# Kernel tuning notes

Measured on AMD Instinct MI355X. Metric: run time of the kernel, lower is better.

The kernel has to match this reference:

```python
import jax, jax.numpy as jnp
import numpy as np
import math

N_EMBED = 512
ENC_HEADS = 8
DEC_HEADS = 16          # 2 * config.n_head
HEAD_DIM = N_EMBED // DEC_HEADS  # 32
N_LAYER = 2
N_MELS = 80
N_AUDIO_CTX = 750
N_TEXT_CTX = 448
VOCAB = 51865
OPT_VOCAB = (VOCAB + 63) // 64 * 64  # 51904
PAD_ID = 0
B = 4
L = 448


def rms(x, eps=1e-6):
    return x * jax.lax.rsqrt(jnp.mean(x * x, axis=-1, keepdims=True) + eps)


def _rotary_tables(T, hd, base=10000.0):
    inv = 1.0 / (base ** (np.arange(0, hd, 2, dtype=np.float64) / hd))
    f = np.arange(T, dtype=np.float64)[:, None] * inv[None, :]
    cos = np.cos(f)[None, :, None, :].astype(np.float32)  # (1,T,1,hd/2)
    sin = np.sin(f)[None, :, None, :].astype(np.float32)
    return jnp.asarray(cos), jnp.asarray(sin)

ROPE_COS, ROPE_SIN = _rotary_tables(10 * N_TEXT_CTX, HEAD_DIM)


def apply_rope(x, cos, sin):
    # x: (b, L, h, hd); cos/sin: (1, L, 1, hd/2)
    d = x.shape[-1] // 2
    x1, x2 = x[..., :d], x[..., d:]
    return jnp.concatenate([x1 * cos + x2 * sin, -x1 * sin + x2 * cos], axis=-1)


def sinusoids(length, channels, max_timescale=10000.0):
    inc = math.log(max_timescale) / (channels // 2 - 1)
    invt = np.exp(-inc * np.arange(channels // 2))
    st = np.arange(length)[:, None] * invt[None, :]
    return jnp.asarray(np.concatenate([np.sin(st), np.cos(st)], axis=1), jnp.float32)

ENC_POS = sinusoids(N_AUDIO_CTX, N_EMBED)


def linear(x, w, b=None):
    y = jnp.einsum('...i,oi->...o', x, w)
    return y + b if b is not None else y


def heads(x, h):
    b, l, _ = x.shape
    return x.reshape(b, l, h, -1).transpose(0, 2, 1, 3)  # (b,h,l,hd)


def conv1d(x, w, b, stride):
    y = jax.lax.conv_general_dilated(x, w, (stride,), [(1, 1)],
                                     dimension_numbers=('NCH', 'OIH', 'NCH'))
    return y + b[None, :, None]


def attn(q, k, v, mask, decorrelate):
    # q,k,v: (b,h,l,hd)
    scale = 1.0 / math.sqrt(q.shape[-1])
    s = jnp.einsum('bhqd,bhkd->bhqk', q, k) * scale
    if mask is not None:
        s = s + mask
    a = jax.nn.softmax(s, axis=-1)
    o = jnp.einsum('bhqk,bhkd->bhqd', a, v)
    if decorrelate:
        # subtract projection of output onto L2-normalized v (self_attn branch)
        vn = v / jnp.maximum(jnp.linalg.norm(v, axis=-1, keepdims=True), 1e-9)
        o = o - jnp.sum(o * vn, axis=-1, keepdims=True) * vn
    b, h, l, d = o.shape
    return o.transpose(0, 2, 1, 3).reshape(b, l, h * d)


def _forward(input_ids, mels, conv1_w, conv1_b, conv2_w, conv2_b,
             enc_qw, enc_qb, enc_kw, enc_kb, enc_vw, enc_vb, enc_ow, enc_ob,
             enc_fcw, enc_fcb, enc_pjw, enc_pjb,
             sqw, sqb, skw, skb, svw, svb, sow, sob,
             cqw, cqb, ckw, ckb, cvw, cvb, cow, cob,
             fcw, fcb, pjw, pjb, embed_w, pos_embed):
    b, Lq = input_ids.shape
    # ---------- audio encoder (Whisper-style convs + custom attn blocks) ----------
    x = jax.nn.gelu(conv1d(mels, conv1_w, conv1_b, 1), approximate=False)
    x = jax.nn.gelu(conv1d(x, conv2_w, conv2_b, 2), approximate=False)
    x = x.transpose(0, 2, 1) + ENC_POS[None]  # (B, n_audio_ctx, n_embed)
    for i in range(N_LAYER):
        h = rms(x)
        q = rms(heads(linear(h, enc_qw[i], enc_qb[i]), ENC_HEADS))
        k = rms(heads(linear(h, enc_kw[i], enc_kb[i]), ENC_HEADS))
        v = heads(linear(h, enc_vw[i], enc_vb[i]), ENC_HEADS)
        x = x + linear(attn(q, k, v, None, True), enc_ow[i], enc_ob[i])
        x = x + linear(jax.nn.gelu(linear(rms(x), enc_fcw[i], enc_fcb[i]), approximate=False),
                       enc_pjw[i], enc_pjb[i])
    aud = rms(x)
    # cross-attn kv projection of audio (no rope)
    aud_k = rms(heads(linear(aud, ckw, ckb), DEC_HEADS))
    aud_v = heads(linear(aud, cvw, cvb), DEC_HEADS)

    # ---------- decoder ----------
    cos, sin = ROPE_COS[:, :Lq], ROPE_SIN[:, :Lq]
    q0 = jnp.broadcast_to(pos_embed[:, :Lq], (b, Lq, N_EMBED))
    ctx = embed_w[input_ids] * math.sqrt(N_EMBED)
    ctx = jnp.concatenate([ctx[:, :1], ctx[:, 1:] + pos_embed[:, :Lq - 1]], axis=1)
    ctx = rms(ctx)

    # self-attn projections: rope then qk-norm; k uses shifted cos/sin
    qh = linear(rms(q0), sqw, sqb).reshape(b, Lq, DEC_HEADS, HEAD_DIM)
    qh = rms(apply_rope(qh, cos, sin).transpose(0, 2, 1, 3))
    k_cos = jnp.concatenate([cos[:, :1], cos[:, :-1]], axis=1)
    k_sin = jnp.concatenate([sin[:, :1], sin[:, :-1]], axis=1)
    kh = linear(ctx, skw, skb).reshape(b, Lq, DEC_HEADS, HEAD_DIM)
    kh = rms(apply_rope(kh, k_cos, k_sin).transpose(0, 2, 1, 3))
    vh = heads(linear(ctx, svw, svb), DEC_HEADS)

    causal = jnp.triu(jnp.full((Lq, Lq), -jnp.inf, jnp.float32), 1)
    kpm = jnp.where(input_ids == PAD_ID, -jnp.inf, 0.0).astype(jnp.float32)
    mask = causal[None, None] + kpm[:, None, None, :]  # (b,1,Lq,Lq)

    res = q0 + linear(attn(qh, kh, vh, mask, True), sow, sob)

    # cross attention (rope on q only, no v-decorrelation)
    q2 = linear(rms(res), cqw, cqb).reshape(b, Lq, DEC_HEADS, HEAD_DIM)
    q2 = rms(apply_rope(q2, cos, sin).transpose(0, 2, 1, 3))
    res = res + linear(attn(q2, aud_k, aud_v, None, False), cow, cob)
    res = res + linear(jax.nn.gelu(linear(rms(res), fcw, fcb), approximate=False), pjw, pjb)

    logits = linear(rms(res), embed_w)  # tied lm head, no bias
    return logits.astype(jnp.float32)


def setup_inputs():
    key = jax.random.key(0)
    ks = iter(jax.random.split(key, 64))
    def w(shape, std=0.02):
        return jax.random.normal(next(ks), shape, jnp.float32) * std
    d = {}
    d['mels'] = jax.random.normal(next(ks), (B, N_MELS, 2 * N_AUDIO_CTX), jnp.float32)
    d['input_ids'] = jax.random.randint(next(ks), (B, L), 1, VOCAB)
    d['conv1_w'] = w((N_EMBED, N_MELS, 3)); d['conv1_b'] = jnp.zeros((N_EMBED,), jnp.float32)
    d['conv2_w'] = w((N_EMBED, N_EMBED, 3)); d['conv2_b'] = jnp.zeros((N_EMBED,), jnp.float32)
    for nm in ['enc_qw', 'enc_kw', 'enc_vw', 'enc_ow']:
        d[nm] = w((N_LAYER, N_EMBED, N_EMBED)); d[nm[:-1] + 'b'] = jnp.zeros((N_LAYER, N_EMBED), jnp.float32)
    d['enc_fcw'] = w((N_LAYER, 4 * N_EMBED, N_EMBED)); d['enc_fcb'] = jnp.zeros((N_LAYER, 4 * N_EMBED), jnp.float32)
    d['enc_pjw'] = w((N_LAYER, N_EMBED, 4 * N_EMBED)); d['enc_pjb'] = jnp.zeros((N_LAYER, N_EMBED), jnp.float32)
    for nm in ['sqw', 'skw', 'svw', 'sow', 'cqw', 'ckw', 'cvw', 'cow']:
        d[nm] = w((N_EMBED, N_EMBED)); d[nm[:-1] + 'b'] = jnp.zeros((N_EMBED,), jnp.float32)
    d['fcw'] = w((4 * N_EMBED, N_EMBED)); d['fcb'] = jnp.zeros((4 * N_EMBED,), jnp.float32)
    d['pjw'] = w((N_EMBED, 4 * N_EMBED)); d['pjb'] = jnp.zeros((N_EMBED,), jnp.float32)
    d['embed_w'] = w((OPT_VOCAB, N_EMBED))
    d['pos_embed'] = jax.random.normal(next(ks), (1, N_TEXT_CTX, N_EMBED), jnp.float32)
    return d


def reference(mels, input_ids, conv1_w, conv1_b, conv2_w, conv2_b,
              enc_qw, enc_qb, enc_kw, enc_kb, enc_vw, enc_vb, enc_ow, enc_ob,
              enc_fcw, enc_fcb, enc_pjw, enc_pjb,
              sqw, sqb, skw, skb, svw, svb, sow, sob,
              cqw, cqb, ckw, ckb, cvw, cvb, cow, cob,
              fcw, fcb, pjw, pjb, embed_w, pos_embed):
    return _forward(input_ids, mels, conv1_w, conv1_b, conv2_w, conv2_b,
                    enc_qw, enc_qb, enc_kw, enc_kb, enc_vw, enc_vb, enc_ow, enc_ob,
                    enc_fcw, enc_fcb, enc_pjw, enc_pjb,
                    sqw, sqb, skw, skb, svw, svb, sow, sob,
                    cqw, cqb, ckw, ckb, cvw, cvb, cow, cob,
                    fcw, fcb, pjw, pjb, embed_w, pos_embed)
```

## Files before the change

### kernel.cpp

```cpp
#include <hip/hip_runtime.h>
#include <math.h>

#define CDIV(a,b) (((a)+(b)-1)/(b))

static constexpr int NE  = 512;
static constexpr int EH  = 8;
static constexpr int EHD = 64;
static constexpr int DHN = 16;
static constexpr int HDD = 32;
static constexpr int NM  = 80;
static constexpr int TMl = 1500;
static constexpr int TP  = 1502;
static constexpr int TA  = 750;
static constexpr int LQ  = 448;
static constexpr int NB  = 4;
static constexpr int OV  = 51904;

typedef __attribute__((ext_vector_type(8))) short bf16x8;
typedef __attribute__((ext_vector_type(8))) unsigned short us8;
typedef __attribute__((ext_vector_type(4))) float f32x4;


__global__ void k_transpose_mels(const float* __restrict__ mels, float* __restrict__ melsT) {
    long idx = (long)blockIdx.x * blockDim.x + threadIdx.x;
    long total = (long)NB * TP * NM;
    if (idx >= total) return;
    int ci = (int)(idx % NM);
    int t  = (int)((idx / NM) % TP);
    int b  = (int)(idx / ((long)NM * TP));
    float v = 0.f;
    if (t >= 1 && t <= TMl) v = mels[((long)b * NM + ci) * TMl + (t - 1)];
    melsT[idx] = v;
}

__global__ void k_zero_x1t_pads(float* __restrict__ x1t) {
    int idx = blockIdx.x * blockDim.x + threadIdx.x;
    if (idx >= NB * 2 * NE) return;
    int c = idx % NE;
    int r = (idx / NE) % 2;
    int b = idx / (NE * 2);
    int t = r ? (TP - 1) : 0;
    x1t[((long)b * TP + t) * NE + c] = 0.f;
}

__global__ void k_repack_w(const float* __restrict__ w, float* __restrict__ wr, int O, int I) {
    long idx = (long)blockIdx.x * blockDim.x + threadIdx.x;
    long total = (long)O * I * 3;
    if (idx >= total) return;
    int k = (int)(idx % 3);
    int i = (int)((idx / 3) % I);
    int o = (int)(idx / ((long)3 * I));
    wr[(long)o * (3 * I) + k * I + i] = w[idx];
}

__global__ void k_add_encpos(float* __restrict__ x) {
    long idx = (long)blockIdx.x * blockDim.x + threadIdx.x;
    long total = (long)NB * TA * NE;
    if (idx >= total) return;
    int c = (int)(idx % NE);
    int t = (int)((idx / NE) % TA);
    double inc = log(10000.0) / 255.0;
    int j = c & 255;
    double st = (double)t * exp(-inc * (double)j);
    float p = (c < 256) ? (float)sin(st) : (float)cos(st);
    x[idx] += p;
}

__global__ void k_embed(const int* __restrict__ ids, const float* __restrict__ ew,
                        const float* __restrict__ pos, float* __restrict__ ctx) {
    long idx = (long)blockIdx.x * blockDim.x + threadIdx.x;
    long total = (long)NB * LQ * NE;
    if (idx >= total) return;
    int c = (int)(idx % NE);
    int t = (int)((idx / NE) % LQ);
    int b = (int)(idx / ((long)NE * LQ));
    int id = ids[b * LQ + t];
    float v = ew[(long)id * NE + c] * 22.62741699796952f;
    if (t >= 1) v += pos[(long)(t - 1) * NE + c];
    ctx[idx] = v;
}

__global__ void k_bcast_pos(const float* __restrict__ pos, float* __restrict__ dst, int Bn) {
    long idx = (long)blockIdx.x * blockDim.x + threadIdx.x;
    long total = (long)Bn * LQ * NE;
    if (idx >= total) return;
    int c = (int)(idx % NE);
    int t = (int)((idx / NE) % LQ);
    dst[idx] = pos[(long)t * NE + c];
}

__global__ void k_ropetab(float* __restrict__ ctab, float* __restrict__ stab) {
    int idx = blockIdx.x * blockDim.x + threadIdx.x;
    if (idx >= LQ * 16) return;
    int m = idx % 16;
    int t = idx / 16;
    double inv = pow(10000.0, -(double)(2 * m) / 32.0);
    double f = (double)t * inv;
    ctab[idx] = (float)cos(f);
    stab[idx] = (float)sin(f);
}

__global__ void k_rope(float* __restrict__ x, int Bn, int shiftK, int RS,
                       const float* __restrict__ ctab, const float* __restrict__ stab) {
    long idx = (long)blockIdx.x * blockDim.x + threadIdx.x;
    long total = (long)Bn * LQ * DHN * 16;
    if (idx >= total) return;
    int m = (int)(idx % 16);
    int h = (int)((idx / 16) % DHN);
    int t = (int)((idx / (16 * DHN)) % LQ);
    int b = (int)(idx / ((long)16 * DHN * LQ));
    int tt = shiftK ? (t > 0 ? t - 1 : 0) : t;
    float c = ctab[tt * 16 + m];
    float s = stab[tt * 16 + m];
    long base = ((long)b * LQ + t) * RS + h * HDD;
    float x1 = x[base + m];
    float x2 = x[base + 16 + m];
    x[base + m]      = x1 * c + x2 * s;
    x[base + 16 + m] = -x1 * s + x2 * c;
}


__global__ void k_rms512(const float* __restrict__ src, float* __restrict__ dst, int rows) {
    int wave = blockIdx.x * (blockDim.x >> 6) + (threadIdx.x >> 6);
    int lane = threadIdx.x & 63;
    if (wave >= rows) return;
    const float* s = src + (long)wave * NE;
    float4 a = *(const float4*)(s + lane * 4);
    float4 b = *(const float4*)(s + 256 + lane * 4);
    float ss = a.x*a.x + a.y*a.y + a.z*a.z + a.w*a.w
             + b.x*b.x + b.y*b.y + b.z*b.z + b.w*b.w;
    for (int m = 32; m >= 1; m >>= 1) ss += __shfl_xor(ss, m, 64);
    float sc = rsqrtf(ss / 512.f + 1e-6f);
    float* d = dst + (long)wave * NE;
    a.x *= sc; a.y *= sc; a.z *= sc; a.w *= sc;
    b.x *= sc; b.y *= sc; b.z *= sc; b.w *= sc;
    *(float4*)(d + lane * 4) = a;
    *(float4*)(d + 256 + lane * 4) = b;
}

template<int D>
__global__ void k_rms_heads(float* __restrict__ x, long nchunks, int CU, int RS) {
    const int RPW = 64 / D;
    long wave = (long)blockIdx.x * (blockDim.x >> 6) + (threadIdx.x >> 6);
    int lane = threadIdx.x & 63;
    long rr = wave * RPW + lane / D;
    if (rr >= nchunks) return;
    int col = lane % D;
    long idx = (rr / CU) * (long)RS + (rr % CU) * D + col;
    float v = x[idx];
    float ss = v * v;
    for (int m = D / 2; m >= 1; m >>= 1) ss += __shfl_xor(ss, m, 64);
    x[idx] = v * rsqrtf(ss / (float)D + 1e-6f);
}

template<int D>
__global__ void k_decorrelate(float* __restrict__ o, const float* __restrict__ v,
                              long nchunks, int CU, int vRS, int vOff) {
    const int RPW = 64 / D;
    long wave = (long)blockIdx.x * (blockDim.x >> 6) + (threadIdx.x >> 6);
    int lane = threadIdx.x & 63;
    long rr = wave * RPW + lane / D;
    if (rr >= nchunks) return;
    int col = lane % D;
    long oidx = rr * D + col;
    long vidx = (rr / CU) * (long)vRS + vOff + (rr % CU) * D + col;
    float ov = o[oidx];
    float vv = v[vidx];
    float dov = ov * vv;
    float dvv = vv * vv;
    for (int m = D / 2; m >= 1; m >>= 1) {
        dov += __shfl_xor(dov, m, 64);
        dvv += __shfl_xor(dvv, m, 64);
    }
    float nv = sqrtf(dvv);
    float c = fmaxf(nv, 1e-9f);
    o[oidx] = ov - (dov / (c * c)) * vv;
}

__global__ void k_softmax(float* __restrict__ s, int H, int Lq, int Lk,
                          int causal, const int* __restrict__ ids, long nrows) {
    long row = (long)blockIdx.x * (blockDim.x >> 6) + (threadIdx.x >> 6);
    if (row >= nrows) return;
    int lane = threadIdx.x & 63;
    int qt = (int)(row % Lq);
    long z = row / Lq;
    int b = (int)(z / H);
    float* p = s + row * (long)Lk;
    int cnt = (Lk + 63) >> 6;
    float vals[12];
    float mx = -INFINITY;
    for (int i = 0; i < cnt; i++) {
        int k = lane + (i << 6);
        float v = -INFINITY;
        if (k < Lk) {
            v = p[k];
            if (causal && k > qt) v = -INFINITY;
            if (ids && ids[(long)b * Lk + k] == 0) v = -INFINITY;
        }
        vals[i] = v;
        mx = fmaxf(mx, v);
    }
    for (int m = 32; m >= 1; m >>= 1) mx = fmaxf(mx, __shfl_xor(mx, m, 64));
    float sum = 0.f;
    for (int i = 0; i < cnt; i++) {
        float e = expf(vals[i] - mx);
        vals[i] = e;
        sum += e;
    }
    for (int m = 32; m >= 1; m >>= 1) sum += __shfl_xor(sum, m, 64);
    float inv = 1.f / sum;
    for (int i = 0; i < cnt; i++) {
        int k = lane + (i << 6);
        if (k < Lk) p[k] = vals[i] * inv;
    }
}


template<bool TRANSB>
__global__ __launch_bounds__(256) void k_gemm(
    const float* __restrict__ A, const float* __restrict__ Bm,
    const float* __restrict__ bias, float* __restrict__ C,
    int M, int N, int K, int lda, int ldb, int ldc,
    long sAb, long sAh, long sBb, long sBh, long sCb, long sCh, int H,
    float alpha, float beta, int act)
{
    __shared__ __align__(16) float As[16][68];
    __shared__ __align__(16) float Bs[16][68];
    int z = blockIdx.z;
    int bb = z / H, hh = z % H;
// ... 79 lines not shown
                                             sAb, sAh, sBb, sBh, sCb, sCh, H, alpha, beta, act);
}


__global__ __launch_bounds__(256, 4) void k_gemm_mf(
    const float* __restrict__ A, const float* __restrict__ B,
    const float* __restrict__ bias, float* __restrict__ C,
    int M, int N, int K, int lda, int ldb, int ldc,
    long sAb, long sAh, long sBb, long sBh, long sCb, long sCh, int H,
    int gx, int gy, float alpha, float beta, int act)
{
    __shared__ __align__(16) unsigned short lds[16384];
    int nwg = gridDim.x;
    int flat = blockIdx.x;
    int q8 = nwg >> 3, r8 = nwg & 7;
    int xcd = flat & 7, idx = flat >> 3;
    int wg = (xcd < r8 ? xcd * (q8 + 1) : r8 * (q8 + 1) + (xcd - r8) * q8) + idx;
    int my = wg % gy;
    int t2 = wg / gy;
    int nx = t2 % gx;
    int z  = t2 / gx;
    int bb = z / H, hh = z % H;
    A += (long)bb * sAb + (long)hh * sAh;
    B += (long)bb * sBb + (long)hh * sBh;
    C += (long)bb * sCb + (long)hh * sCh;
    int m0 = my * 128, n0 = nx * 128;
    const int tid = threadIdx.x;
    const int wid = tid >> 6, lane = tid & 63;
    const int wm = wid >> 1, wn = wid & 1;
    const int lr = lane & 15, lk = lane >> 4;
    const int rA = tid >> 2, g = tid & 3;

    f32x4 acc[4][4] = {};

    for (int k0 = 0; k0 < K; k0 += 32) {
        __syncthreads();
        int kk = k0 + g * 8;
        bool kv = kk < K;
        #pragma unroll
        for (int half = 0; half < 2; ++half) {
            int r = rA + half * 64;
            int off = r * 32 + (g ^ ((r >> 1) & 3)) * 8;
            {
                float4 f0 = {0,0,0,0}, f1 = {0,0,0,0};
                if (kv && m0 + r < M) {
                    const float* p = A + (long)(m0 + r) * lda + kk;
                    f0 = *(const float4*)p;
                    f1 = *(const float4*)(p + 4);
                }
                float ff[8] = {f0.x,f0.y,f0.z,f0.w,f1.x,f1.y,f1.z,f1.w};
                us8 h, l;
                #pragma unroll
                for (int j = 0; j < 8; ++j) {
                    unsigned bu = __float_as_uint(ff[j]);
                    unsigned hb = bu & 0xffff0000u;
                    h[j] = (unsigned short)(hb >> 16);
                    l[j] = (unsigned short)(__float_as_uint(ff[j] - __uint_as_float(hb)) >> 16);
                }
                *(us8*)(lds + off) = h;
                *(us8*)(lds + 4096 + off) = l;
            }
            {
                float4 f0 = {0,0,0,0}, f1 = {0,0,0,0};
                if (kv && n0 + r < N) {
                    const float* p = B + (long)(n0 + r) * ldb + kk;
                    f0 = *(const float4*)p;
                    f1 = *(const float4*)(p + 4);
                }
                float ff[8] = {f0.x,f0.y,f0.z,f0.w,f1.x,f1.y,f1.z,f1.w};
                us8 h, l;
                #pragma unroll
                for (int j = 0; j < 8; ++j) {
                    unsigned bu = __float_as_uint(ff[j]);
                    unsigned hb = bu & 0xffff0000u;
                    h[j] = (unsigned short)(hb >> 16);
                    l[j] = (unsigned short)(__float_as_uint(ff[j] - __uint_as_float(hb)) >> 16);
                }
                *(us8*)(lds + 8192 + off) = h;
                *(us8*)(lds + 12288 + off) = l;
            }
        }
        __syncthreads();
        bf16x8 ah[4], al[4];
        #pragma unroll
        for (int i = 0; i < 4; ++i) {
            int ra = wm * 64 + i * 16 + lr;
            int ao = ra * 32 + (lk ^ ((ra >> 1) & 3)) * 8;
            ah[i] = *(const bf16x8*)(lds + ao);
            al[i] = *(const bf16x8*)(lds + 4096 + ao);
        }
        #pragma unroll
        for (int j = 0; j < 4; ++j) {
            int rb = wn * 64 + j * 16 + lr;
            int bo = rb * 32 + (lk ^ ((rb >> 1) & 3)) * 8;
            bf16x8 bh = *(const bf16x8*)(lds + 8192 + bo);
            bf16x8 bl = *(const bf16x8*)(lds + 12288 + bo);
            #pragma unroll
            for (int i = 0; i < 4; ++i) {
                acc[i][j] = __builtin_amdgcn_mfma_f32_16x16x32_bf16(ah[i], bh, acc[i][j], 0, 0, 0);
                acc[i][j] = __builtin_amdgcn_mfma_f32_16x16x32_bf16(ah[i], bl, acc[i][j], 0, 0, 0);
                acc[i][j] = __builtin_amdgcn_mfma_f32_16x16x32_bf16(al[i], bh, acc[i][j], 0, 0, 0);
            }
        }
    }
    #pragma unroll
    for (int i = 0; i < 4; ++i) {
        int rowb = m0 + wm * 64 + i * 16 + lk * 4;
        #pragma unroll
        for (int j = 0; j < 4; ++j) {
            int col = n0 + wn * 64 + j * 16 + lr;
            if (col >= N) continue;
            float bi = bias ? bias[col] : 0.f;
            #pragma unroll
            for (int qi = 0; qi < 4; ++qi) {
                int row = rowb + qi;
                if (row >= M) continue;
                float v = alpha * acc[i][j][qi] + bi;
                long off = (long)row * ldc + col;
                if (beta != 0.f) v += beta * C[off];
                if (act) v = 0.5f * v * (1.f + erff(v * 0.70710678118654752f));
                C[off] = v;
            }
        }
    }
}

static inline void gemm_mf(hipStream_t st, const float* A, const float* B, const float* bias,
                           float* C, int M, int N, int K, int lda, int ldb, int ldc,
                           long sAb, long sAh, long sBb, long sBh, long sCb, long sCh,
                           int Z, int H, float alpha, float beta, int act)
{
    int gx = CDIV(N, 128), gy = CDIV(M, 128);
    dim3 g((unsigned)(gx * gy * Z));
    k_gemm_mf<<<g, 256, 0, st>>>(A, B, bias, C, M, N, K, lda, ldb, ldc,
                                 sAb, sAh, sBb, sBh, sCb, sCh, H, gx, gy, alpha, beta, act);
}


extern "C" void kernel_launch(void* const* d_in, const int* in_sizes, int n_in,
                              void* d_out, int out_size, void* d_ws, size_t ws_size,
                              hipStream_t stream)
{
    const float* mels = (const float*)d_in[0];
    const int*   ids  = (const int*)  d_in[1];
    const float* c1w  = (const float*)d_in[2];
    const float* c1b  = (const float*)d_in[3];
    const float* c2w  = (const float*)d_in[4];
    const float* c2b  = (const float*)d_in[5];
    const float* eqw  = (const float*)d_in[6];
    const float* eqb  = (const float*)d_in[7];
    const float* ekw  = (const float*)d_in[8];
    const float* ekb  = (const float*)d_in[9];
    const float* evw  = (const float*)d_in[10];
    const float* evb  = (const float*)d_in[11];
    const float* eow  = (const float*)d_in[12];
    const float* eob  = (const float*)d_in[13];
    const float* efcw = (const float*)d_in[14];
    const float* efcb = (const float*)d_in[15];
    const float* epjw = (const float*)d_in[16];
    const float* epjb = (const float*)d_in[17];
    const float* sqw  = (const float*)d_in[18];
    const float* sqb  = (const float*)d_in[19];
    const float* skw  = (const float*)d_in[20];
    const float* skb  = (const float*)d_in[21];
    const float* svw  = (const float*)d_in[22];
    const float* svb  = (const float*)d_in[23];
    const float* soww = (const float*)d_in[24];
    const float* sob  = (const float*)d_in[25];
    const float* cqw  = (const float*)d_in[26];
    const float* cqb  = (const float*)d_in[27];
    const float* ckw  = (const float*)d_in[28];
    const float* ckb  = (const float*)d_in[29];
    const float* cvw  = (const float*)d_in[30];
    const float* cvb  = (const float*)d_in[31];
    const float* coww = (const float*)d_in[32];
    const float* cob  = (const float*)d_in[33];
    const float* fcw  = (const float*)d_in[34];
    const float* fcb  = (const float*)d_in[35];
    const float* pjw  = (const float*)d_in[36];
    const float* pjb  = (const float*)d_in[37];
    const float* embw = (const float*)d_in[38];
    const float* pose = (const float*)d_in[39];
    float* out = (float*)d_out;

    float* ws = (float*)d_ws;
    long off = 0;
    auto alloc = [&](long n) { float* p = ws + off; off += n; return p; };
    float* melsT = alloc((long)NB * TP * NM);
    float* x1t   = alloc((long)NB * TP * NE);
    float* w1r   = alloc(3L * NE * NM);
    float* w2r   = alloc(3L * NE * NE);
    float* xenc  = alloc((long)NB * TA * NE);
    float* hbuf  = alloc((long)NB * TA * NE);
    float* qbuf  = alloc((long)NB * TA * NE);
    float* kbuf  = alloc((long)NB * TA * NE);
    float* vbuf  = alloc((long)NB * TA * NE);
    float* obuf  = alloc((long)NB * TA * NE);
    float* fcbuf = alloc((long)NB * TA * 2048);
    float* sc    = alloc((long)NB * DHN * LQ * TA);
    float* audk  = alloc((long)NB * TA * NE);
    float* audv  = alloc((long)NB * TA * NE);
    float* ctx   = alloc((long)NB * LQ * NE);
    float* q0r   = alloc((long)LQ * NE);
    float* qh    = alloc((long)NB * LQ * NE);
    float* kh    = alloc((long)NB * LQ * NE);
    float* vh    = alloc((long)NB * LQ * NE);
    float* res   = alloc((long)NB * LQ * NE);
    float* t1    = alloc((long)NB * LQ * NE);
    float* odec  = alloc((long)NB * LQ * NE);
    float* ctab  = alloc((long)LQ * 16);
    float* stab  = alloc((long)LQ * 16);
    float* cbias = alloc(2048);
    (void)ws_size; (void)in_sizes; (void)n_in; (void)out_size;
    (void)qbuf; (void)kbuf; (void)vbuf; (void)audk; (void)audv; (void)kh; (void)vh;

    const int MA = NB * TA;
    const int MD = NB * LQ;
    const float dscale = 0.17677669529663687f;

    float* selfkv = fcbuf;
    float* audkv  = fcbuf + 3000000L;

    auto dcopy = [&](float* dst, const float* src, long n) {
        hipMemcpyAsync(dst, src, n * sizeof(float), hipMemcpyDeviceToDevice, stream);
    };

    k_transpose_mels<<<CDIV((long)NB * TP * NM, 256), 256, 0, stream>>>(mels, melsT);
    k_repack_w<<<CDIV(3L * NE * NM, 256), 256, 0, stream>>>(c1w, w1r, NE, NM);
    k_repack_w<<<CDIV(3L * NE * NE, 256), 256, 0, stream>>>(c2w, w2r, NE, NE);
    k_zero_x1t_pads<<<CDIV(NB * 2 * NE, 256), 256, 0, stream>>>(x1t);
    gemm_mf(stream, melsT, w1r, c1b, x1t + NE,
            TMl, NE, 3 * NM, NM, 3 * NM, NE,
            (long)TP * NM, 0, 0, 0, (long)TP * NE, 0, NB, 1, 1.f, 0.f, 1);
    gemm_mf(stream, x1t, w2r, c2b, xenc,
            TA, NE, 3 * NE, 2 * NE, 3 * NE, NE,
            (long)TP * NE, 0, 0, 0, (long)TA * NE, 0, NB, 1, 1.f, 0.f, 1);
    k_add_encpos<<<CDIV((long)NB * TA * NE, 256), 256, 0, stream>>>(xenc);

    for (int l = 0; l < 2; l++) {
        const float* qw = eqw + (long)l * NE * NE; const float* qb = eqb + l * NE;
        const float* kw = ekw + (long)l * NE * NE; const float* kb = ekb + l * NE;
        const float* vw = evw + (long)l * NE * NE; const float* vb = evb + l * NE;
        const float* ow = eow + (long)l * NE * NE; const float* ob = eob + l * NE;
        const float* fw = efcw + (long)l * 2048 * NE; const float* fb = efcb + l * 2048;
        const float* pw = epjw + (long)l * NE * 2048; const float* pb = epjb + l * NE;

        dcopy(w2r,                   qw, (long)NE * NE);
        dcopy(w2r + (long)NE * NE,   kw, (long)NE * NE);
        dcopy(w2r + 2L * NE * NE,    vw, (long)NE * NE);
        dcopy(cbias,        qb, NE);
        dcopy(cbias + NE,   kb, NE);
        dcopy(cbias + 2*NE, vb, NE);

        k_rms512<<<CDIV(MA, 4), 256, 0, stream>>>(xenc, hbuf, MA);
        gemm_mf(stream, hbuf, w2r, cbias, fcbuf, MA, 3 * NE, NE, NE, NE, 3 * NE,
                0,0,0,0,0,0, 1,1, 1.f, 0.f, 0);
        k_rms_heads<64><<<CDIV((long)MA * 16, 4), 256, 0, stream>>>(fcbuf, (long)MA * 16, 16, 3 * NE);
        gemm_mf(stream, fcbuf, fcbuf + NE, nullptr, sc, TA, TA, EHD, 3 * NE, 3 * NE, TA,
                (long)TA * 3 * NE, EHD, (long)TA * 3 * NE, EHD, (long)EH * TA * TA, (long)TA * TA,
                NB * EH, EH, 0.125f, 0.f, 0);
        k_softmax<<<CDIV((long)NB * EH * TA, 4), 256, 0, stream>>>(sc, EH, TA, TA, 0, nullptr, (long)NB * EH * TA);
        gemm(stream, false, sc, fcbuf + 2 * NE, nullptr, obuf, TA, EHD, TA, TA, 3 * NE, NE,
             (long)EH * TA * TA, (long)TA * TA, (long)TA * 3 * NE, EHD, (long)TA * NE, EHD,
             NB * EH, EH, 1.f, 0.f, 0);
        k_decorrelate<64><<<CDIV((long)MA * EH, 4), 256, 0, stream>>>(obuf, fcbuf + 2 * NE, (long)MA * EH, EH, 3 * NE, 0);
        gemm_mf(stream, obuf, ow, ob, xenc, MA, NE, NE, NE, NE, NE, 0,0,0,0,0,0, 1,1, 1.f, 1.f, 0);

        k_rms512<<<CDIV(MA, 4), 256, 0, stream>>>(xenc, hbuf, MA);
        gemm_mf(stream, hbuf, fw, fb, fcbuf, MA, 2048, NE, NE, NE, 2048, 0,0,0,0,0,0, 1,1, 1.f, 0.f, 1);
        gemm_mf(stream, fcbuf, pw, pb, xenc, MA, NE, 2048, 2048, 2048, NE, 0,0,0,0,0,0, 1,1, 1.f, 1.f, 0);
    }

    dcopy(w2r,                 ckw, (long)NE * NE);
    dcopy(w2r + (long)NE * NE, cvw, (long)NE * NE);
    dcopy(cbias,      ckb, NE);
    dcopy(cbias + NE, cvb, NE);
    k_rms512<<<CDIV(MA, 4), 256, 0, stream>>>(xenc, hbuf, MA);
    gemm_mf(stream, hbuf, w2r, cbias, audkv, MA, 2 * NE, NE, NE, NE, 2 * NE,
            0,0,0,0,0,0, 1,1, 1.f, 0.f, 0);
    k_rms_heads<32><<<CDIV((long)MA * DHN, 8), 256, 0, stream>>>(audkv, (long)MA * DHN, DHN, 2 * NE);

    k_embed<<<CDIV((long)NB * LQ * NE, 256), 256, 0, stream>>>(ids, embw, pose, ctx);
    k_rms512<<<CDIV(MD, 4), 256, 0, stream>>>(ctx, ctx, MD);
    k_ropetab<<<CDIV(LQ * 16, 256), 256, 0, stream>>>(ctab, stab);

    k_bcast_pos<<<CDIV((long)LQ * NE, 256), 256, 0, stream>>>(pose, q0r, 1);
    k_rms512<<<CDIV(LQ, 4), 256, 0, stream>>>(q0r, q0r, LQ);
    gemm_mf(stream, q0r, sqw, sqb, qh, LQ, NE, NE, NE, NE, NE, 0,0,0,0,0,0, 1,1, 1.f, 0.f, 0);
    k_rope<<<CDIV((long)LQ * DHN * 16, 256), 256, 0, stream>>>(qh, 1, 0, NE, ctab, stab);
    k_rms_heads<32><<<CDIV((long)LQ * DHN, 8), 256, 0, stream>>>(qh, (long)LQ * DHN, DHN, NE);

    dcopy(w2r,                 skw, (long)NE * NE);
    dcopy(w2r + (long)NE * NE, svw, (long)NE * NE);
    dcopy(cbias,      skb, NE);
    dcopy(cbias + NE, svb, NE);
    gemm_mf(stream, ctx, w2r, cbias, selfkv, MD, 2 * NE, NE, NE, NE, 2 * NE,
            0,0,0,0,0,0, 1,1, 1.f, 0.f, 0);
    k_rope<<<CDIV((long)NB * LQ * DHN * 16, 256), 256, 0, stream>>>(selfkv, NB, 1, 2 * NE, ctab, stab);
    k_rms_heads<32><<<CDIV((long)MD * DHN, 8), 256, 0, stream>>>(selfkv, (long)MD * DHN, DHN, 2 * NE);

    gemm_mf(stream, qh, selfkv, nullptr, sc, LQ, LQ, HDD, NE, 2 * NE, LQ,
            0, HDD, (long)LQ * 2 * NE, HDD, (long)DHN * LQ * LQ, (long)LQ * LQ,
            NB * DHN, DHN, dscale, 0.f, 0);
    k_softmax<<<CDIV((long)NB * DHN * LQ, 4), 256, 0, stream>>>(sc, DHN, LQ, LQ, 1, ids, (long)NB * DHN * LQ);
    gemm(stream, false, sc, selfkv + NE, nullptr, odec, LQ, HDD, LQ, LQ, 2 * NE, NE,
         (long)DHN * LQ * LQ, (long)LQ * LQ, (long)LQ * 2 * NE, HDD, (long)LQ * NE, HDD,
         NB * DHN, DHN, 1.f, 0.f, 0);
    k_decorrelate<32><<<CDIV((long)MD * DHN, 8), 256, 0, stream>>>(odec, selfkv + NE, (long)MD * DHN, DHN, 2 * NE, 0);
    k_bcast_pos<<<CDIV((long)NB * LQ * NE, 256), 256, 0, stream>>>(pose, res, NB);
    gemm_mf(stream, odec, soww, sob, res, MD, NE, NE, NE, NE, NE, 0,0,0,0,0,0, 1,1, 1.f, 1.f, 0);

    k_rms512<<<CDIV(MD, 4), 256, 0, stream>>>(res, t1, MD);
    gemm_mf(stream, t1, cqw, cqb, qh, MD, NE, NE, NE, NE, NE, 0,0,0,0,0,0, 1,1, 1.f, 0.f, 0);
    k_rope<<<CDIV((long)NB * LQ * DHN * 16, 256), 256, 0, stream>>>(qh, NB, 0, NE, ctab, stab);
    k_rms_heads<32><<<CDIV((long)MD * DHN, 8), 256, 0, stream>>>(qh, (long)MD * DHN, DHN, NE);
    gemm_mf(stream, qh, audkv, nullptr, sc, LQ, TA, HDD, NE, 2 * NE, TA,
            (long)LQ * NE, HDD, (long)TA * 2 * NE, HDD, (long)DHN * LQ * TA, (long)LQ * TA,
            NB * DHN, DHN, dscale, 0.f, 0);
    k_softmax<<<CDIV((long)NB * DHN * LQ, 4), 256, 0, stream>>>(sc, DHN, LQ, TA, 0, nullptr, (long)NB * DHN * LQ);
    gemm(stream, false, sc, audkv + NE, nullptr, odec, LQ, HDD, TA, TA, 2 * NE, NE,
         (long)DHN * LQ * TA, (long)LQ * TA, (long)TA * 2 * NE, HDD, (long)LQ * NE, HDD,
         NB * DHN, DHN, 1.f, 0.f, 0);
    gemm_mf(stream, odec, coww, cob, res, MD, NE, NE, NE, NE, NE, 0,0,0,0,0,0, 1,1, 1.f, 1.f, 0);

    k_rms512<<<CDIV(MD, 4), 256, 0, stream>>>(res, t1, MD);
    gemm_mf(stream, t1, fcw, fcb, fcbuf, MD, 2048, NE, NE, NE, 2048, 0,0,0,0,0,0, 1,1, 1.f, 0.f, 1);
    gemm_mf(stream, fcbuf, pjw, pjb, res, MD, NE, 2048, 2048, 2048, NE, 0,0,0,0,0,0, 1,1, 1.f, 1.f, 0);

    k_rms512<<<CDIV(MD, 4), 256, 0, stream>>>(res, t1, MD);
    gemm_mf(stream, t1, embw, nullptr, out, MD, OV, NE, NE, NE, OV,
            0,0,0,0,0,0, 1,1, 1.f, 0.f, 0);
}
```

Baseline: 3.214 ms.

## Pre-split operands into bf16 hi/lo buffers and add a split-input GEMM

```diff
diff --git a/kernel.cpp b/kernel.cpp
--- a/kernel.cpp
+++ b/kernel.cpp
@@ -20,8 +20,17 @@
 typedef __attribute__((ext_vector_type(8))) unsigned short us8;
 typedef __attribute__((ext_vector_type(4))) float f32x4;
 
-
-__global__ void k_transpose_mels(const float* __restrict__ mels, float* __restrict__ melsT) {
+__device__ __forceinline__ void split1(float f, unsigned short& h, unsigned short& l) {
+    unsigned bu = __float_as_uint(f);
+    unsigned hb = bu & 0xffff0000u;
+    h = (unsigned short)(hb >> 16);
+    l = (unsigned short)(__float_as_uint(f - __uint_as_float(hb)) >> 16);
+}
+
+
+__global__ void k_transpose_mels_s(const float* __restrict__ mels,
+                                   unsigned short* __restrict__ hi,
+                                   unsigned short* __restrict__ lo) {
     long idx = (long)blockIdx.x * blockDim.x + threadIdx.x;
     long total = (long)NB * TP * NM;
     if (idx >= total) return;
@@ -30,27 +39,33 @@
     int b  = (int)(idx / ((long)NM * TP));
     float v = 0.f;
     if (t >= 1 && t <= TMl) v = mels[((long)b * NM + ci) * TMl + (t - 1)];
-    melsT[idx] = v;
-}
-
-__global__ void k_zero_x1t_pads(float* __restrict__ x1t) {
+    unsigned short h, l; split1(v, h, l);
+    hi[idx] = h; lo[idx] = l;
+}
+
+__global__ void k_zero_x1t_pads_s(unsigned short* __restrict__ hi, unsigned short* __restrict__ lo) {
     int idx = blockIdx.x * blockDim.x + threadIdx.x;
     if (idx >= NB * 2 * NE) return;
     int c = idx % NE;
     int r = (idx / NE) % 2;
     int b = idx / (NE * 2);
     int t = r ? (TP - 1) : 0;
-    x1t[((long)b * TP + t) * NE + c] = 0.f;
-}
-
-__global__ void k_repack_w(const float* __restrict__ w, float* __restrict__ wr, int O, int I) {
+    long o = ((long)b * TP + t) * NE + c;
+    hi[o] = 0; lo[o] = 0;
+}
+
+__global__ void k_repack_w_s(const float* __restrict__ w,
+                             unsigned short* __restrict__ hi, unsigned short* __restrict__ lo,
+                             int O, int I) {
     long idx = (long)blockIdx.x * blockDim.x + threadIdx.x;
     long total = (long)O * I * 3;
     if (idx >= total) return;
     int k = (int)(idx % 3);
     int i = (int)((idx / 3) % I);
     int o = (int)(idx / ((long)3 * I));
-    wr[(long)o * (3 * I) + k * I + i] = w[idx];
+    unsigned short h, l; split1(w[idx], h, l);
+    long d = (long)o * (3 * I) + k * I + i;
+    hi[d] = h; lo[d] = l;
 }
 
 __global__ void k_add_encpos(float* __restrict__ x) {
@@ -120,7 +135,9 @@
 }
 
 
-__global__ void k_rms512(const float* __restrict__ src, float* __restrict__ dst, int rows) {
+__global__ void k_rms512s(const float* __restrict__ src,
+                          unsigned short* __restrict__ hi, unsigned short* __restrict__ lo,
+                          int rows) {
     int wave = blockIdx.x * (blockDim.x >> 6) + (threadIdx.x >> 6);
     int lane = threadIdx.x & 63;
     if (wave >= rows) return;
@@ -131,11 +148,18 @@
              + b.x*b.x + b.y*b.y + b.z*b.z + b.w*b.w;
     for (int m = 32; m >= 1; m >>= 1) ss += __shfl_xor(ss, m, 64);
     float sc = rsqrtf(ss / 512.f + 1e-6f);
-    float* d = dst + (long)wave * NE;
-    a.x *= sc; a.y *= sc; a.z *= sc; a.w *= sc;
-    b.x *= sc; b.y *= sc; b.z *= sc; b.w *= sc;
-    *(float4*)(d + lane * 4) = a;
-    *(float4*)(d + 256 + lane * 4) = b;
+    float fa[4] = {a.x*sc, a.y*sc, a.z*sc, a.w*sc};
+    float fb[4] = {b.x*sc, b.y*sc, b.z*sc, b.w*sc};
+    ushort4 ha, la, hb, lb;
+    split1(fa[0], ha.x, la.x); split1(fa[1], ha.y, la.y);
+    split1(fa[2], ha.z, la.z); split1(fa[3], ha.w, la.w);
+    split1(fb[0], hb.x, lb.x); split1(fb[1], hb.y, lb.y);
+    split1(fb[2], hb.z, lb.z); split1(fb[3], hb.w, lb.w);
+    long base = (long)wave * NE;
+    *(ushort4*)(hi + base + lane * 4) = ha;
+    *(ushort4*)(lo + base + lane * 4) = la;
+    *(ushort4*)(hi + base + 256 + lane * 4) = hb;
+    *(ushort4*)(lo + base + 256 + lane * 4) = lb;
 }
 
 template<int D>
@@ -154,8 +178,9 @@
 }
 
 template<int D>
-__global__ void k_decorrelate(float* __restrict__ o, const float* __restrict__ v,
-                              long nchunks, int CU, int vRS, int vOff) {
+__global__ void k_decorr_s(const float* __restrict__ o, const float* __restrict__ v,
+                           unsigned short* __restrict__ hi, unsigned short* __restrict__ lo,
+                           long nchunks, int CU, int vRS, int vOff) {
     const int RPW = 64 / D;
     long wave = (long)blockIdx.x * (blockDim.x >> 6) + (threadIdx.x >> 6);
     int lane = threadIdx.x & 63;
@@ -174,7 +199,22 @@
     }
     float nv = sqrtf(dvv);
     float c = fmaxf(nv, 1e-9f);
-    o[oidx] = ov - (dov / (c * c)) * vv;
+    float res = ov - (dov / (c * c)) * vv;
+    unsigned short h, l; split1(res, h, l);
+    hi[oidx] = h; lo[oidx] = l;
+}
+
+__global__ void k_split(const float* __restrict__ x, unsigned short* __restrict__ hi,
+                        unsigned short* __restrict__ lo, long n4)
+{
+    long i = (long)blockIdx.x * blockDim.x + threadIdx.x;
+    if (i >= n4) return;
+    float4 v = ((const float4*)x)[i];
+    ushort4 h, l;
+    split1(v.x, h.x, l.x); split1(v.y, h.y, l.y);
+    split1(v.z, h.z, l.z); split1(v.w, h.w, l.w);
+    ((ushort4*)hi)[i] = h;
+    ((ushort4*)lo)[i] = l;
 }
 
 __global__ void k_softmax(float* __restrict__ s, int H, int Lq, int Lk,
@@ -360,10 +400,8 @@
                 us8 h, l;
                 #pragma unroll
                 for (int j = 0; j < 8; ++j) {
-                    unsigned bu = __float_as_uint(ff[j]);
-                    unsigned hb = bu & 0xffff0000u;
-                    h[j] = (unsigned short)(hb >> 16);
-                    l[j] = (unsigned short)(__float_as_uint(ff[j] - __uint_as_float(hb)) >> 16);
+                    unsigned short hh2, ll2; split1(ff[j], hh2, ll2);
+                    h[j] = hh2; l[j] = ll2;
                 }
                 *(us8*)(lds + off) = h;
                 *(us8*)(lds + 4096 + off) = l;
@@ -379,10 +417,8 @@
                 us8 h, l;
                 #pragma unroll
                 for (int j = 0; j < 8; ++j) {
-                    unsigned bu = __float_as_uint(ff[j]);
-                    unsigned hb = bu & 0xffff0000u;
-                    h[j] = (unsigned short)(hb >> 16);
-                    l[j] = (unsigned short)(__float_as_uint(ff[j] - __uint_as_float(hb)) >> 16);
+                    unsigned short hh2, ll2; split1(ff[j], hh2, ll2);
+                    h[j] = hh2; l[j] = ll2;
                 }
                 *(us8*)(lds + 8192 + off) = h;
                 *(us8*)(lds + 12288 + off) = l;
@@ -442,6 +478,125 @@
     dim3 g((unsigned)(gx * gy * Z));
     k_gemm_mf<<<g, 256, 0, st>>>(A, B, bias, C, M, N, K, lda, ldb, ldc,
                                  sAb, sAh, sBb, sBh, sCb, sCh, H, gx, gy, alpha, beta, act);
+}
+
+
+__global__ __launch_bounds__(256, 4) void k_gemm_bs(
+    const unsigned short* __restrict__ Ah, const unsigned short* __restrict__ Al,
+    const unsigned short* __restrict__ Bh, const unsigned short* __restrict__ Bl,
+    const float* __restrict__ bias, float* __restrict__ C,
+    unsigned short* __restrict__ Chi, unsigned short* __restrict__ Clo,
+    int M, int N, int K, int lda, int ldb, int ldc,
+    long sAb, long sCb, int gx, int gy, float beta, int act, int osplit)
+{
+    __shared__ __align__(16) unsigned short lds[16384];
+    int nwg = gridDim.x;
+    int flat = blockIdx.x;
+    int q8 = nwg >> 3, r8 = nwg & 7;
+    int xcd = flat & 7, idx = flat >> 3;
+    int wg = (xcd < r8 ? xcd * (q8 + 1) : r8 * (q8 + 1) + (xcd - r8) * q8) + idx;
+    int my = wg % gy;
+    int t2 = wg / gy;
+    int nx = t2 % gx;
+    int bb = t2 / gx;
+    Ah += (long)bb * sAb; Al += (long)bb * sAb;
+    int m0 = my * 128, n0 = nx * 128;
+    const int tid = threadIdx.x;
+    const int wid = tid >> 6, lane = tid & 63;
+    const int wm = wid >> 1, wn = wid & 1;
+    const int lr = lane & 15, lk = lane >> 4;
+    const int rA = tid >> 2, g = tid & 3;
+
+    f32x4 acc[4][4] = {};
+
+    for (int k0 = 0; k0 < K; k0 += 32) {
+        __syncthreads();
+        int kk = k0 + g * 8;
+        bool kv = kk < K;
+        #pragma unroll
+        for (int half = 0; half < 2; ++half) {
+            int r = rA + half * 64;
+            int off = r * 32 + (g ^ ((r >> 1) & 3)) * 8;
+            us8 vh = {0,0,0,0,0,0,0,0}, vl = {0,0,0,0,0,0,0,0};
+            if (kv && m0 + r < M) {
+                long ao = (long)(m0 + r) * lda + kk;
+                vh = *(const us8*)(Ah + ao);
+                vl = *(const us8*)(Al + ao);
+            }
+            *(us8*)(lds + off) = vh;
+            *(us8*)(lds + 4096 + off) = vl;
+            us8 wh = {0,0,0,0,0,0,0,0}, wl = {0,0,0,0,0,0,0,0};
+            if (kv && n0 + r < N) {
+                long bo = (long)(n0 + r) * ldb + kk;
+                wh = *(const us8*)(Bh + bo);
+                wl = *(const us8*)(Bl + bo);
+            }
+            *(us8*)(lds + 8192 + off) = wh;
+            *(us8*)(lds + 12288 + off) = wl;
+        }
+        __syncthreads();
+        bf16x8 ah[4], al[4];
+        #pragma unroll
+        for (int i = 0; i < 4; ++i) {
+            int ra = wm * 64 + i * 16 + lr;
+            int ao = ra * 32 + (lk ^ ((ra >> 1) & 3)) * 8;
+            ah[i] = *(const bf16x8*)(lds + ao);
+            al[i] = *(const bf16x8*)(lds + 4096 + ao);
+        }
+        #pragma unroll
+        for (int j = 0; j < 4; ++j) {
+            int rb = wn * 64 + j * 16 + lr;
+            int bo = rb * 32 + (lk ^ ((rb >> 1) & 3)) * 8;
+            bf16x8 bh = *(const bf16x8*)(lds + 8192 + bo);
+            bf16x8 bl = *(const bf16x8*)(lds + 12288 + bo);
+            #pragma unroll
+            for (int i = 0; i < 4; ++i) {
+                acc[i][j] = __builtin_amdgcn_mfma_f32_16x16x32_bf16(ah[i], bh, acc[i][j], 0, 0, 0);
+                acc[i][j] = __builtin_amdgcn_mfma_f32_16x16x32_bf16(ah[i], bl, acc[i][j], 0, 0, 0);
+                acc[i][j] = __builtin_amdgcn_mfma_f32_16x16x32_bf16(al[i], bh, acc[i][j], 0, 0, 0);
+            }
+        }
+    }
+    #pragma unroll
+    for (int i = 0; i < 4; ++i) {
+        int rowb = m0 + wm * 64 + i * 16 + lk * 4;
+        #pragma unroll
+        for (int j = 0; j < 4; ++j) {
+            int col = n0 + wn * 64 + j * 16 + lr;
+            if (col >= N) continue;
+            float bi = bias ? bias[col] : 0.f;
+            #pragma unroll
+            for (int qi = 0; qi < 4; ++qi) {
+                int row = rowb + qi;
+                if (row >= M) continue;
+                float v = acc[i][j][qi] + bi;
+                long off2 = (long)bb * sCb + (long)row * ldc + col;
+                if (osplit) {
+                    if (act) v = 0.5f * v * (1.f + erff(v * 0.70710678118654752f));
+                    unsigned short h, l; split1(v, h, l);
+                    Chi[off2] = h; Clo[off2] = l;
+                } else {
+                    if (beta != 0.f) v += beta * C[off2];
+                    if (act) v = 0.5f * v * (1.f + erff(v * 0.70710678118654752f));
+                    C[off2] = v;
+                }
+            }
+        }
+    }
+}
+
+static inline void gemm_bs(hipStream_t st,
+                           const unsigned short* Ah, const unsigned short* Al,
+                           const unsigned short* Bh, const unsigned short* Bl,
+                           const float* bias, float* C,
+                           unsigned short* Chi, unsigned short* Clo,
+                           int M, int N, int K, int lda, int ldb, int ldc,
+                           long sAb, long sCb, int Z, float beta, int act, int osplit)
+{
+    int gx = CDIV(N, 128), gy = CDIV(M, 128);
+    dim3 g((unsigned)(gx * gy * Z));
+    k_gemm_bs<<<g, 256, 0, st>>>(Ah, Al, Bh, Bl, bias, C, Chi, Clo,
+                                 M, N, K, lda, ldb, ldc, sAb, sCb, gx, gy, beta, act, osplit);
 }
 
 
@@ -520,29 +675,47 @@
     float* stab  = alloc((long)LQ * 16);
     float* cbias = alloc(2048);
     (void)ws_size; (void)in_sizes; (void)n_in; (void)out_size;
-    (void)qbuf; (void)kbuf; (void)vbuf; (void)audk; (void)audv; (void)kh; (void)vh;
+    (void)vbuf; (void)audk; (void)audv; (void)t1;
 
     const int MA = NB * TA;
     const int MD = NB * LQ;
     const float dscale = 0.17677669529663687f;
 
+    typedef unsigned short us;
+    us* melH = (us*)melsT;              us* melL = melH + (long)NB * TP * NM;
+    us* x1H  = (us*)x1t;                us* x1L  = x1H + (long)NB * TP * NE;
+    us* w1H  = (us*)w1r;                us* w1L  = w1H + 3L * NE * NM;
+    us* w2H  = (us*)w2r;                us* w2L  = w2H + 3L * NE * NE;
+    us* hspH = (us*)hbuf;               us* hspL = hspH + (long)MA * NE;
+    us* ospH = (us*)qbuf;               us* ospL = ospH + (long)MA * NE;
+    us* bspH = (us*)kbuf;               us* bspL = bspH + 1048576L;
+    us* cspH = (us*)vh;                 us* cspL = cspH + (long)MD * NE;
+    us* dspH = (us*)kh;                 us* dspL = dspH + (long)MD * NE;
+    const long EMW = (long)OV * NE;
+    us* embH = (us*)ws;                 us* embL = embH + EMW;
     float* selfkv = fcbuf;
     float* audkv  = fcbuf + 3000000L;
-
+    us* fcsH = (us*)fcbuf;
+
+    auto split = [&](const float* x, long n, us* hi, us* lo) {
+        k_split<<<dim3((unsigned)CDIV(n / 4, 256)), 256, 0, stream>>>(x, hi, lo, n / 4);
+    };
     auto dcopy = [&](float* dst, const float* src, long n) {
         hipMemcpyAsync(dst, src, n * sizeof(float), hipMemcpyDeviceToDevice, stream);
     };
-
-    k_transpose_mels<<<CDIV((long)NB * TP * NM, 256), 256, 0, stream>>>(mels, melsT);
-    k_repack_w<<<CDIV(3L * NE * NM, 256), 256, 0, stream>>>(c1w, w1r, NE, NM);
-    k_repack_w<<<CDIV(3L * NE * NE, 256), 256, 0, stream>>>(c2w, w2r, NE, NE);
-    k_zero_x1t_pads<<<CDIV(NB * 2 * NE, 256), 256, 0, stream>>>(x1t);
-    gemm_mf(stream, melsT, w1r, c1b, x1t + NE,
+    const long nW = (long)NE * NE;
+    const long nFC = 2048L * NE;
+
+    k_transpose_mels_s<<<CDIV((long)NB * TP * NM, 256), 256, 0, stream>>>(mels, melH, melL);
+    k_repack_w_s<<<CDIV(3L * NE * NM, 256), 256, 0, stream>>>(c1w, w1H, w1L, NE, NM);
+    k_repack_w_s<<<CDIV(3L * NE * NE, 256), 256, 0, stream>>>(c2w, w2H, w2L, NE, NE);
+    k_zero_x1t_pads_s<<<CDIV(NB * 2 * NE, 256), 256, 0, stream>>>(x1H, x1L);
+    gemm_bs(stream, melH, melL, w1H, w1L, c1b, nullptr, x1H + NE, x1L + NE,
             TMl, NE, 3 * NM, NM, 3 * NM, NE,
-            (long)TP * NM, 0, 0, 0, (long)TP * NE, 0, NB, 1, 1.f, 0.f, 1);
-    gemm_mf(stream, x1t, w2r, c2b, xenc,
+            (long)TP * NM, (long)TP * NE, NB, 0.f, 1, 1);
+    gemm_bs(stream, x1H, x1L, w2H, w2L, c2b, xenc, nullptr, nullptr,
             TA, NE, 3 * NE, 2 * NE, 3 * NE, NE,
-            (long)TP * NE, 0, 0, 0, (long)TA * NE, 0, NB, 1, 1.f, 0.f, 1);
+            (long)TP * NE, (long)TA * NE, NB, 0.f, 1, 0);
     k_add_encpos<<<CDIV((long)NB * TA * NE, 256), 256, 0, stream>>>(xenc);
 
     for (int l = 0; l < 2; l++) {
@@ -553,16 +726,16 @@
         const float* fw = efcw + (long)l * 2048 * NE; const float* fb = efcb + l * 2048;
         const float* pw = epjw + (long)l * NE * 2048; const float* pb = epjb + l * NE;
 
-        dcopy(w2r,                   qw, (long)NE * NE);
-        dcopy(w2r + (long)NE * NE,   kw, (long)NE * NE);
-        dcopy(w2r + 2L * NE * NE,    vw, (long)NE * NE);
+        split(qw, nW, bspH,          bspL);
+        split(kw, nW, bspH + nW,     bspL + nW);
+        split(vw, nW, bspH + 2 * nW, bspL + 2 * nW);
         dcopy(cbias,        qb, NE);
         dcopy(cbias + NE,   kb, NE);
         dcopy(cbias + 2*NE, vb, NE);
 
-        k_rms512<<<CDIV(MA, 4), 256, 0, stream>>>(xenc, hbuf, MA);
-        gemm_mf(stream, hbuf, w2r, cbias, fcbuf, MA, 3 * NE, NE, NE, NE, 3 * NE,
-                0,0,0,0,0,0, 1,1, 1.f, 0.f, 0);
+        k_rms512s<<<CDIV(MA, 4), 256, 0, stream>>>(xenc, hspH, hspL, MA);
+        gemm_bs(stream, hspH, hspL, bspH, bspL, cbias, fcbuf, nullptr, nullptr,
+                MA, 3 * NE, NE, NE, NE, 3 * NE, 0, 0, 1, 0.f, 0, 0);
         k_rms_heads<64><<<CDIV((long)MA * 16, 4), 256, 0, stream>>>(fcbuf, (long)MA * 16, 16, 3 * NE);
         gemm_mf(stream, fcbuf, fcbuf + NE, nullptr, sc, TA, TA, EHD, 3 * NE, 3 * NE, TA,
                 (long)TA * 3 * NE, EHD, (long)TA * 3 * NE, EHD, (long)EH * TA * TA, (long)TA * TA,
@@ -571,39 +744,48 @@
         gemm(stream, false, sc, fcbuf + 2 * NE, nullptr, obuf, TA, EHD, TA, TA, 3 * NE, NE,
              (long)EH * TA * TA, (long)TA * TA, (long)TA * 3 * NE, EHD, (long)TA * NE, EHD,
              NB * EH, EH, 1.f, 0.f, 0);
-        k_decorrelate<64><<<CDIV((long)MA * EH, 4), 256, 0, stream>>>(obuf, fcbuf + 2 * NE, (long)MA * EH, EH, 3 * NE, 0);
-        gemm_mf(stream, obuf, ow, ob, xenc, MA, NE, NE, NE, NE, NE, 0,0,0,0,0,0, 1,1, 1.f, 1.f, 0);
-
-        k_rms512<<<CDIV(MA, 4), 256, 0, stream>>>(xenc, hbuf, MA);
-        gemm_mf(stream, hbuf, fw, fb, fcbuf, MA, 2048, NE, NE, NE, 2048, 0,0,0,0,0,0, 1,1, 1.f, 0.f, 1);
-        gemm_mf(stream, fcbuf, pw, pb, xenc, MA, NE, 2048, 2048, 2048, NE, 0,0,0,0,0,0, 1,1, 1.f, 1.f, 0);
-    }
-
-    dcopy(w2r,                 ckw, (long)NE * NE);
-    dcopy(w2r + (long)NE * NE, cvw, (long)NE * NE);
+        k_decorr_s<64><<<CDIV((long)MA * EH, 4), 256, 0, stream>>>(obuf, fcbuf + 2 * NE, ospH, ospL,
+                                                                   (long)MA * EH, EH, 3 * NE, 0);
+        split(ow, nW, bspH, bspL);
+        gemm_bs(stream, ospH, ospL, bspH, bspL, ob, xenc, nullptr, nullptr,
+                MA, NE, NE, NE, NE, NE, 0, 0, 1, 1.f, 0, 0);
+
+        k_rms512s<<<CDIV(MA, 4), 256, 0, stream>>>(xenc, hspH, hspL, MA);
+        split(fw, nFC, bspH, bspL);
+        gemm_bs(stream, hspH, hspL, bspH, bspL, fb, nullptr, fcsH, fcsH + (long)MA * 2048,
+                MA, 2048, NE, NE, NE, 2048, 0, 0, 1, 0.f, 1, 1);
+        split(pw, nFC, bspH, bspL);
+        gemm_bs(stream, fcsH, fcsH + (long)MA * 2048, bspH, bspL, pb, xenc, nullptr, nullptr,
+                MA, NE, 2048, 2048, 2048, NE, 0, 0, 1, 1.f, 0, 0);
+    }
+
+    split(ckw, nW, bspH,      bspL);
+    split(cvw, nW, bspH + nW, bspL + nW);
     dcopy(cbias,      ckb, NE);
     dcopy(cbias + NE, cvb, NE);
-    k_rms512<<<CDIV(MA, 4), 256, 0, stream>>>(xenc, hbuf, MA);
-    gemm_mf(stream, hbuf, w2r, cbias, audkv, MA, 2 * NE, NE, NE, NE, 2 * NE,
-            0,0,0,0,0,0, 1,1, 1.f, 0.f, 0);
+    k_rms512s<<<CDIV(MA, 4), 256, 0, stream>>>(xenc, hspH, hspL, MA);
+    gemm_bs(stream, hspH, hspL, bspH, bspL, cbias, audkv, nullptr, nullptr,
+            MA, 2 * NE, NE, NE, NE, 2 * NE, 0, 0, 1, 0.f, 0, 0);
     k_rms_heads<32><<<CDIV((long)MA * DHN, 8), 256, 0, stream>>>(audkv, (long)MA * DHN, DHN, 2 * NE);
 
     k_embed<<<CDIV((long)NB * LQ * NE, 256), 256, 0, stream>>>(ids, embw, pose, ctx);
-    k_rms512<<<CDIV(MD, 4), 256, 0, stream>>>(ctx, ctx, MD);
+    k_rms512s<<<CDIV(MD, 4), 256, 0, stream>>>(ctx, cspH, cspL, MD);
     k_ropetab<<<CDIV(LQ * 16, 256), 256, 0, stream>>>(ctab, stab);
 
     k_bcast_pos<<<CDIV((long)LQ * NE, 256), 256, 0, stream>>>(pose, q0r, 1);
-    k_rms512<<<CDIV(LQ, 4), 256, 0, stream>>>(q0r, q0r, LQ);
-    gemm_mf(stream, q0r, sqw, sqb, qh, LQ, NE, NE, NE, NE, NE, 0,0,0,0,0,0, 1,1, 1.f, 0.f, 0);
+    k_rms512s<<<CDIV(LQ, 4), 256, 0, stream>>>(q0r, dspH, dspL, LQ);
+    split(sqw, nW, bspH, bspL);
+    gemm_bs(stream, dspH, dspL, bspH, bspL, sqb, qh, nullptr, nullptr,
+            LQ, NE, NE, NE, NE, NE, 0, 0, 1, 0.f, 0, 0);
     k_rope<<<CDIV((long)LQ * DHN * 16, 256), 256, 0, stream>>>(qh, 1, 0, NE, ctab, stab);
     k_rms_heads<32><<<CDIV((long)LQ * DHN, 8), 256, 0, stream>>>(qh, (long)LQ * DHN, DHN, NE);
 
-    dcopy(w2r,                 skw, (long)NE * NE);
-    dcopy(w2r + (long)NE * NE, svw, (long)NE * NE);
+    split(skw, nW, bspH,      bspL);
+    split(svw, nW, bspH + nW, bspL + nW);
     dcopy(cbias,      skb, NE);
     dcopy(cbias + NE, svb, NE);
-    gemm_mf(stream, ctx, w2r, cbias, selfkv, MD, 2 * NE, NE, NE, NE, 2 * NE,
-            0,0,0,0,0,0, 1,1, 1.f, 0.f, 0);
+    gemm_bs(stream, cspH, cspL, bspH, bspL, cbias, selfkv, nullptr, nullptr,
+            MD, 2 * NE, NE, NE, NE, 2 * NE, 0, 0, 1, 0.f, 0, 0);
     k_rope<<<CDIV((long)NB * LQ * DHN * 16, 256), 256, 0, stream>>>(selfkv, NB, 1, 2 * NE, ctab, stab);
     k_rms_heads<32><<<CDIV((long)MD * DHN, 8), 256, 0, stream>>>(selfkv, (long)MD * DHN, DHN, 2 * NE);
 
@@ -614,12 +796,17 @@
     gemm(stream, false, sc, selfkv + NE, nullptr, odec, LQ, HDD, LQ, LQ, 2 * NE, NE,
          (long)DHN * LQ * LQ, (long)LQ * LQ, (long)LQ * 2 * NE, HDD, (long)LQ * NE, HDD,
          NB * DHN, DHN, 1.f, 0.f, 0);
-    k_decorrelate<32><<<CDIV((long)MD * DHN, 8), 256, 0, stream>>>(odec, selfkv + NE, (long)MD * DHN, DHN, 2 * NE, 0);
+    k_decorr_s<32><<<CDIV((long)MD * DHN, 8), 256, 0, stream>>>(odec, selfkv + NE, dspH, dspL,
+                                                                (long)MD * DHN, DHN, 2 * NE, 0);
     k_bcast_pos<<<CDIV((long)NB * LQ * NE, 256), 256, 0, stream>>>(pose, res, NB);
-    gemm_mf(stream, odec, soww, sob, res, MD, NE, NE, NE, NE, NE, 0,0,0,0,0,0, 1,1, 1.f, 1.f, 0);
-
-    k_rms512<<<CDIV(MD, 4), 256, 0, stream>>>(res, t1, MD);
-    gemm_mf(stream, t1, cqw, cqb, qh, MD, NE, NE, NE, NE, NE, 0,0,0,0,0,0, 1,1, 1.f, 0.f, 0);
+    split(soww, nW, bspH, bspL);
+    gemm_bs(stream, dspH, dspL, bspH, bspL, sob, res, nullptr, nullptr,
+            MD, NE, NE, NE, NE, NE, 0, 0, 1, 1.f, 0, 0);
+
+    k_rms512s<<<CDIV(MD, 4), 256, 0, stream>>>(res, cspH, cspL, MD);
+    split(cqw, nW, bspH, bspL);
+    gemm_bs(stream, cspH, cspL, bspH, bspL, cqb, qh, nullptr, nullptr,
+            MD, NE, NE, NE, NE, NE, 0, 0, 1, 0.f, 0, 0);
     k_rope<<<CDIV((long)NB * LQ * DHN * 16, 256), 256, 0, stream>>>(qh, NB, 0, NE, ctab, stab);
     k_rms_heads<32><<<CDIV((long)MD * DHN, 8), 256, 0, stream>>>(qh, (long)MD * DHN, DHN, NE);
     gemm_mf(stream, qh, audkv, nullptr, sc, LQ, TA, HDD, NE, 2 * NE, TA,
@@ -629,13 +816,21 @@
     gemm(stream, false, sc, audkv + NE, nullptr, odec, LQ, HDD, TA, TA, 2 * NE, NE,
          (long)DHN * LQ * TA, (long)LQ * TA, (long)TA * 2 * NE, HDD, (long)LQ * NE, HDD,
          NB * DHN, DHN, 1.f, 0.f, 0);
-    gemm_mf(stream, odec, coww, cob, res, MD, NE, NE, NE, NE, NE, 0,0,0,0,0,0, 1,1, 1.f, 1.f, 0);
-
-    k_rms512<<<CDIV(MD, 4), 256, 0, stream>>>(res, t1, MD);
-    gemm_mf(stream, t1, fcw, fcb, fcbuf, MD, 2048, NE, NE, NE, 2048, 0,0,0,0,0,0, 1,1, 1.f, 0.f, 1);
-    gemm_mf(stream, fcbuf, pjw, pjb, res, MD, NE, 2048, 2048, 2048, NE, 0,0,0,0,0,0, 1,1, 1.f, 1.f, 0);
-
-    k_rms512<<<CDIV(MD, 4), 256, 0, stream>>>(res, t1, MD);
-    gemm_mf(stream, t1, embw, nullptr, out, MD, OV, NE, NE, NE, OV,
-            0,0,0,0,0,0, 1,1, 1.f, 0.f, 0);
-}
+    split(odec, (long)MD * NE, dspH, dspL);
+    split(coww, nW, bspH, bspL);
+    gemm_bs(stream, dspH, dspL, bspH, bspL, cob, res, nullptr, nullptr,
+            MD, NE, NE, NE, NE, NE, 0, 0, 1, 1.f, 0, 0);
+
+    k_rms512s<<<CDIV(MD, 4), 256, 0, stream>>>(res, cspH, cspL, MD);
+    split(fcw, nFC, bspH, bspL);
+    gemm_bs(stream, cspH, cspL, bspH, bspL, fcb, nullptr, fcsH, fcsH + (long)MD * 2048,
+            MD, 2048, NE, NE, NE, 2048, 0, 0, 1, 0.f, 1, 1);
+    split(pjw, nFC, bspH, bspL);
+    gemm_bs(stream, fcsH, fcsH + (long)MD * 2048, bspH, bspL, pjb, res, nullptr, nullptr,
+            MD, NE, 2048, 2048, 2048, NE, 0, 0, 1, 1.f, 0, 0);
+
+    k_rms512s<<<CDIV(MD, 4), 256, 0, stream>>>(res, cspH, cspL, MD);
+    split(embw, EMW, embH, embL);
+    gemm_bs(stream, cspH, cspL, embH, embL, nullptr, out, nullptr, nullptr,
+            MD, OV, NE, NE, NE, OV, 0, 0, 1, 0.f, 0, 0);
+}
```

Measured after the change: 2.997 ms. 6.7% less time.
